# Performance work log

Hardware: AMD Instinct MI355X
Metric: run time of the kernel (lower is better)

Reference implementation:

```python
import jax, jax.numpy as jnp
import numpy as np

EPS = 1e-3  # keras LayerNormalization default epsilon
H = 12     # number_of_heads


def _layer_norm(x, gamma, beta):
    mu = jnp.mean(x, axis=-1, keepdims=True)
    var = jnp.mean(jnp.square(x - mu), axis=-1, keepdims=True)
    return (x - mu) * jax.lax.rsqrt(var + EPS) * gamma + beta


def _gelu(x):
    return jax.nn.gelu(x, approximate=False)  # keras 'gelu' default is erf-based


def setup_inputs():
    key = jax.random.key(0)
    B, N, E, F, Fe = 8, 1024, 16384, 96, 32
    ks = jax.random.split(key, 20)
    def dense(k, din, dout):
        return jax.random.normal(k, (din, dout), jnp.float32) / np.float32(np.sqrt(din))
    return {
        "nodes": jax.random.normal(ks[0], (B, N, F), jnp.float32),
        "edge_features": jax.random.normal(ks[1], (B, E, Fe), jnp.float32),
        "edges": jax.random.randint(ks[2], (B, E, 2), 0, N),
        "edge_weights": jax.random.uniform(ks[3], (B, E, 1), jnp.float32),
        "edge_dropout": jnp.ones((B, E, 2), jnp.float32),
        # message layer: Dense(F) on concat([src,dst,edge_feat]) + GELU + LayerNorm
        "Wm": dense(ks[4], 2 * F + Fe, F), "bm": jnp.zeros((F,), jnp.float32),
        "gm": jnp.ones((F,), jnp.float32), "betam": jnp.zeros((F,), jnp.float32),
        # gated MHSA on concat([nodes, aggregated]) (2F -> F) + GELU + LayerNorm
        "Wq": dense(ks[5], 2 * F, F), "bq": jnp.zeros((F,), jnp.float32),
        "Wk": dense(ks[6], 2 * F, F), "bk": jnp.zeros((F,), jnp.float32),
        "Wv": dense(ks[7], 2 * F, F), "bv": jnp.zeros((F,), jnp.float32),
        "Wg": dense(ks[8], 2 * F, F), "bg": jnp.zeros((F,), jnp.float32),
        "Wo": dense(ks[9], F, F), "bo": jnp.zeros((F,), jnp.float32),
        "gu": jnp.ones((F,), jnp.float32), "betau": jnp.zeros((F,), jnp.float32),
    }


def reference(nodes, edge_features, edges, edge_weights, edge_dropout,
              Wm, bm, gm, betam, Wq, bq, Wk, bk, Wv, bv, Wg, bg, Wo, bo, gu, betau):
    B, N, F = nodes.shape
    E = edges.shape[1]
    # gather both endpoint features per edge: [B, E, 2F]
    gathered = jnp.take_along_axis(nodes, edges.reshape(B, 2 * E, 1), axis=1)
    msg_in = jnp.concatenate([gathered.reshape(B, E, 2 * F), edge_features], axis=-1)
    messages = _layer_norm(_gelu(msg_in @ Wm + bm), gm, betam)        # [B,E,F]
    weighted_messages = messages * edge_weights                        # [B,E,F]
    # batched scatter-sum onto target node edges[...,1], gated by dropout[...,1]
    contrib = weighted_messages * edge_dropout[..., 1:2]
    seg_ids = (edges[..., 1] + jnp.arange(B, dtype=edges.dtype)[:, None] * N).reshape(-1)
    aggregated = jax.ops.segment_sum(contrib.reshape(B * E, F), seg_ids,
                                     num_segments=B * N).reshape(B, N, F)
    # gated multi-head self-attention over concat(nodes, aggregated)
    x = jnp.concatenate([nodes, aggregated], axis=-1)                  # [B,N,2F]
    d = F // H
    def split_heads(y):
        return y.reshape(B, N, H, d).transpose(0, 2, 1, 3)             # [B,H,N,d]
    q = split_heads(x @ Wq + bq)
    k = split_heads(x @ Wk + bk)
    v = split_heads(x @ Wv + bv)
    gate = jax.nn.sigmoid(split_heads(x @ Wg + bg))
    scores = jnp.einsum("bhqd,bhkd->bhqk", q, k) / jnp.sqrt(jnp.float32(d))
    att = jnp.einsum("bhqk,bhkd->bhqd", jax.nn.softmax(scores, axis=-1), v) * gate
    att = att.transpose(0, 2, 1, 3).reshape(B, N, F)
    updated_nodes = _layer_norm(_gelu(att @ Wo + bo), gu, betau)
    return updated_nodes, weighted_messages, edges, edge_weights, edge_dropout
```

## Files before the change

### kernel.cpp

```cpp
#include <hip/hip_runtime.h>
#include <hip/hip_bf16.h>

#define BB 8
#define NN 1024
#define EE 16384
#define FF 96
#define FE 32
#define NH 12
#define DD 8
#define KM 224
#define KX 192
#define TE 64
#define BK 32

__device__ __forceinline__ float gelu_erf(float x){
    return 0.5f * x * (1.0f + erff(x * 0.70710678118654752f));
}

__device__ __forceinline__ int load_idx(const int* __restrict__ p, int i){
    int v = p[i];
    if (!((unsigned)v < 1024u)) v = (int)__int_as_float(v);
    return min(max(v, 0), NN-1);
}

__global__ __launch_bounds__(256) void hist_kernel(
    const int* __restrict__ edges, int* __restrict__ cnt)
{
    const int i = blockIdx.x*blockDim.x + threadIdx.x;
    if (i < BB*EE){
        const int b = i >> 14;
        const int dst = load_idx(edges, 2*i+1);
        atomicAdd(&cnt[b*NN + dst], 1);
    }
}

__global__ __launch_bounds__(1024) void scan_kernel(
    const int* __restrict__ cnt, int* __restrict__ rowstart, int* __restrict__ cursor)
{
    const int b = blockIdx.x;
    const int t = threadIdx.x;
    __shared__ int s[NN];
    const int v = cnt[b*NN + t];
    s[t] = v;
    __syncthreads();
    for (int off = 1; off < NN; off <<= 1){
        int u = (t >= off) ? s[t-off] : 0;
        __syncthreads();
        s[t] += u;
        __syncthreads();
    }
    const int ex = s[t] - v + b*EE;
    rowstart[b*NN + t] = ex;
    cursor[b*NN + t]   = ex;
}

__global__ __launch_bounds__(256) void scatter_kernel(
    const int* __restrict__ edges, int* __restrict__ cursor, int* __restrict__ elist)
{
    const int i = blockIdx.x*blockDim.x + threadIdx.x;
    if (i < BB*EE){
        const int b = i >> 14;
        const int dst = load_idx(edges, 2*i+1);
        const int pos = atomicAdd(&cursor[b*NN + dst], 1);
        elist[pos] = i;
    }
}

__global__ __launch_bounds__(256) void node_proj_kernel(
    const float* __restrict__ nodes, const float* __restrict__ Wm,
    float* __restrict__ P1, float* __restrict__ P2)
{
    const int rt  = blockIdx.x;
    const int m   = blockIdx.y;
    const int tid = threadIdx.x;
    const int tx  = tid & 15;
    const int ty  = tid >> 4;
    const int r0  = rt * TE;

    const float* W = Wm + (size_t)(m ? FF : 0) * FF;
    float* out     = m ? P2 : P1;

    __shared__ float Xs[TE][BK+4];
    __shared__ float Ws[BK][FF];

    float acc[4][6];
    #pragma unroll
    for (int a=0;a<4;++a)
        #pragma unroll
        for (int c=0;c<6;++c) acc[a][c] = 0.f;

    const int e_st = tid >> 2;
    const int kk0  = (tid & 3) * 8;

    for (int c = 0; c < 3; ++c){
        __syncthreads();
        {
            const float4* src = (const float4*)(W + (size_t)c*BK*FF);
            float4* dst = (float4*)&Ws[0][0];
            dst[tid      ] = src[tid      ];
            dst[tid + 256] = src[tid + 256];
            dst[tid + 512] = src[tid + 512];
        }
        {
            const float* rp = nodes + (size_t)(r0 + e_st)*FF + c*BK;
            *(float4*)&Xs[e_st][kk0    ] = *(const float4*)(rp + kk0);
            *(float4*)&Xs[e_st][kk0 + 4] = *(const float4*)(rp + kk0 + 4);
        }
        __syncthreads();
        #pragma unroll 4
        for (int kk = 0; kk < BK; ++kk){
            float2 w01 = *(const float2*)&Ws[kk][6*tx    ];
            float2 w23 = *(const float2*)&Ws[kk][6*tx + 2];
            float2 w45 = *(const float2*)&Ws[kk][6*tx + 4];
            float xv[4];
            #pragma unroll
            for (int ei=0; ei<4; ++ei) xv[ei] = Xs[ty + 16*ei][kk];
            #pragma unroll
            for (int ei=0; ei<4; ++ei){
                acc[ei][0] += xv[ei]*w01.x;  acc[ei][1] += xv[ei]*w01.y;
                acc[ei][2] += xv[ei]*w23.x;  acc[ei][3] += xv[ei]*w23.y;
                acc[ei][4] += xv[ei]*w45.x;  acc[ei][5] += xv[ei]*w45.y;
            }
        }
    }

    #pragma unroll
    for (int ei = 0; ei < 4; ++ei){
        const int row = r0 + ty + 16*ei;
        float* __restrict__ orow = out + (size_t)row*FF + 6*tx;
        #pragma unroll
        for (int jj=0; jj<6; ++jj) orow[jj] = acc[ei][jj];
    }
}

__global__ __launch_bounds__(256) void edge_msg2_kernel(
    const float* __restrict__ P1, const float* __restrict__ P2,
    const float* __restrict__ ef,
    const int*  __restrict__ edges, const float* __restrict__ ew,
    const float* __restrict__ Wm, const float* __restrict__ bm,
    const float* __restrict__ gm, const float* __restrict__ betam,
    float* __restrict__ wm_out)
{
    const int bid = blockIdx.x;
    const int tid = threadIdx.x;
    const int tx  = tid & 15;
    const int ty  = tid >> 4;
    const int be0 = bid * TE;
    const int b   = be0 >> 14;

    __shared__ float Xs[TE][BK+4];
    __shared__ float Ws[BK][FF];
    __shared__ int   eidx[TE*2];
    __shared__ float ewS[TE];
    __shared__ float bmS[FF], gmS[FF], betamS[FF];

    if (tid < TE*2){
        int v = edges[(size_t)be0*2 + tid];
        if (!((unsigned)v < 1024u)) v = (int)__int_as_float(v);
        eidx[tid] = min(max(v, 0), NN-1);
    }
    if (tid < TE) ewS[tid] = ew[be0 + tid];
    if (tid < FF){ bmS[tid] = bm[tid]; gmS[tid] = gm[tid]; betamS[tid] = betam[tid]; }

    float acc[4][6];
    #pragma unroll
    for (int a=0;a<4;++a)
        #pragma unroll
        for (int c=0;c<6;++c) acc[a][c] = 0.f;

    const int e_st = tid >> 2;
    const int kk0  = (tid & 3) * 8;

    {
        const float4* src = (const float4*)(Wm + (size_t)KX*FF);
        float4* dst = (float4*)&Ws[0][0];
        dst[tid      ] = src[tid      ];
        dst[tid + 256] = src[tid + 256];
        dst[tid + 512] = src[tid + 512];
    }
    {
        const float* rp = ef + (size_t)(be0 + e_st)*FE;
        *(float4*)&Xs[e_st][kk0    ] = *(const float4*)(rp + kk0);
        *(float4*)&Xs[e_st][kk0 + 4] = *(const float4*)(rp + kk0 + 4);
    }
    __syncthreads();
    #pragma unroll 4
    for (int kk = 0; kk < BK; ++kk){
        float2 w01 = *(const float2*)&Ws[kk][6*tx    ];
        float2 w23 = *(const float2*)&Ws[kk][6*tx + 2];
        float2 w45 = *(const float2*)&Ws[kk][6*tx + 4];
        float xv[4];
        #pragma unroll
        for (int ei=0; ei<4; ++ei) xv[ei] = Xs[ty + 16*ei][kk];
        #pragma unroll
        for (int ei=0; ei<4; ++ei){
            acc[ei][0] += xv[ei]*w01.x;  acc[ei][1] += xv[ei]*w01.y;
            acc[ei][2] += xv[ei]*w23.x;  acc[ei][3] += xv[ei]*w23.y;
            acc[ei][4] += xv[ei]*w45.x;  acc[ei][5] += xv[ei]*w45.y;
        }
    }

    float add[4][6];
    #pragma unroll
    for (int ei = 0; ei < 4; ++ei){
        const int el = ty + 16*ei;
        const int sn = eidx[2*el];
        const int dn = eidx[2*el+1];
        const float2* p1 = (const float2*)(P1 + (size_t)(b*NN + sn)*FF + 6*tx);
        const float2* p2 = (const float2*)(P2 + (size_t)(b*NN + dn)*FF + 6*tx);
        const float2 a0 = p1[0], a1 = p1[1], a2 = p1[2];
        const float2 b0 = p2[0], b1 = p2[1], b2 = p2[2];
        add[ei][0] = a0.x + b0.x;  add[ei][1] = a0.y + b0.y;
        add[ei][2] = a1.x + b1.x;  add[ei][3] = a1.y + b1.y;
        add[ei][4] = a2.x + b2.x;  add[ei][5] = a2.y + b2.y;
    }

    #pragma unroll
    for (int ei = 0; ei < 4; ++ei){
        const int el = ty + 16*ei;
        float h[6]; float psum = 0.f;
        #pragma unroll
        for (int jj=0; jj<6; ++jj){
            h[jj] = gelu_erf(acc[ei][jj] + add[ei][jj] + bmS[6*tx + jj]);
            psum += h[jj];
        }
        #pragma unroll
        for (int m=1; m<16; m<<=1) psum += __shfl_xor(psum, m, 16);
        const float mu = psum * (1.f/FF);
        float vsum = 0.f;
        #pragma unroll
        for (int jj=0; jj<6; ++jj){ float d = h[jj]-mu; vsum += d*d; }
        #pragma unroll
        for (int m=1; m<16; m<<=1) vsum += __shfl_xor(vsum, m, 16);
        const float rstd = rsqrtf(vsum*(1.f/FF) + 1e-3f);

        const float w = ewS[el];
        float* __restrict__ wrow = wm_out + (size_t)(be0 + el)*FF + 6*tx;
        #pragma unroll
        for (int jj=0; jj<6; ++jj)
            wrow[jj] = ((h[jj]-mu)*rstd*gmS[6*tx+jj] + betamS[6*tx+jj]) * w;
    }
}

__global__ __launch_bounds__(96) void gather_kernel(
    const float* __restrict__ wm_out, const float* __restrict__ ed,
    const int* __restrict__ elist, const int* __restrict__ rowstart,
    const int* __restrict__ cnt, float* __restrict__ agg)
{
    const int bn = blockIdx.x;
    const int t  = threadIdx.x;
    const int beg = rowstart[bn];
    const int num = cnt[bn];
    float sum = 0.f;
    for (int i = 0; i < num; ++i){
        const int be = elist[beg + i];
        const float coeff = ed[2*(size_t)be + 1];
        sum += wm_out[(size_t)be*FF + t] * coeff;
    }
    agg[(size_t)bn*FF + t] = sum;
}

__global__ __launch_bounds__(256) void qkvg_kernel(
    const float* __restrict__ nodes, const float* __restrict__ agg,
    const float* __restrict__ Wq, const float* __restrict__ bq,
    const float* __restrict__ Wk, const float* __restrict__ bk,
    const float* __restrict__ Wv, const float* __restrict__ bv,
    const float* __restrict__ Wg, const float* __restrict__ bg,
    float* __restrict__ qo, float* __restrict__ ko,
    float* __restrict__ vo, float* __restrict__ go)
{
    const int rt  = blockIdx.x;
    const int m   = blockIdx.y;
    const int tid = threadIdx.x;
    const int tx  = tid & 15;
    const int ty  = tid >> 4;
    const int r0  = rt * TE;

    const float* W    = (m==0)?Wq:(m==1)?Wk:(m==2)?Wv:Wg;
    const float* bias = (m==0)?bq:(m==1)?bk:(m==2)?bv:bg;
    float* out        = (m==0)?qo:(m==1)?ko:(m==2)?vo:go;

    __shared__ float Xs[TE][BK+4];
    __shared__ float Ws[BK][FF];
    __shared__ float bS[FF];
    if (tid < FF) bS[tid] = bias[tid];

    float acc[4][6];
    #pragma unroll
    for (int a=0;a<4;++a)
        #pragma unroll
        for (int c=0;c<6;++c) acc[a][c] = 0.f;

    const int e_st = tid >> 2;
    const int kk0  = (tid & 3) * 8;

    for (int c = 0; c < 6; ++c){
        __syncthreads();
        {
            const float4* src = (const float4*)(W + (size_t)c*BK*FF);
            float4* dst = (float4*)&Ws[0][0];
            dst[tid      ] = src[tid      ];
            dst[tid + 256] = src[tid + 256];
            dst[tid + 512] = src[tid + 512];
        }
        {
            const float* rp = (c < 3)
                ? nodes + (size_t)(r0 + e_st)*FF + c*BK
                : agg   + (size_t)(r0 + e_st)*FF + (c-3)*BK;
            *(float4*)&Xs[e_st][kk0    ] = *(const float4*)(rp + kk0);
            *(float4*)&Xs[e_st][kk0 + 4] = *(const float4*)(rp + kk0 + 4);
        }
        __syncthreads();
        #pragma unroll 4
        for (int kk = 0; kk < BK; ++kk){
            float2 w01 = *(const float2*)&Ws[kk][6*tx    ];
            float2 w23 = *(const float2*)&Ws[kk][6*tx + 2];
            float2 w45 = *(const float2*)&Ws[kk][6*tx + 4];
            float xv[4];
            #pragma unroll
            for (int ei=0; ei<4; ++ei) xv[ei] = Xs[ty + 16*ei][kk];
            #pragma unroll
            for (int ei=0; ei<4; ++ei){
                acc[ei][0] += xv[ei]*w01.x;  acc[ei][1] += xv[ei]*w01.y;
                acc[ei][2] += xv[ei]*w23.x;  acc[ei][3] += xv[ei]*w23.y;
                acc[ei][4] += xv[ei]*w45.x;  acc[ei][5] += xv[ei]*w45.y;
            }
        }
    }

    #pragma unroll
    for (int ei = 0; ei < 4; ++ei){
        const int row = r0 + ty + 16*ei;
        float* __restrict__ orow = out + (size_t)row*FF + 6*tx;
        #pragma unroll
        for (int jj=0; jj<6; ++jj) orow[jj] = acc[ei][jj] + bS[6*tx + jj];
    }
}

__global__ __launch_bounds__(256) void attn_kernel(
    const float* __restrict__ q, const float* __restrict__ k,
    const float* __restrict__ v, const float* g,
    float* att)
{
    const int blk = blockIdx.x;
    const int qt = blk & 15;
    const int h  = (blk >> 4) % NH;
    const int b  = blk / (16*NH);
    const int tid  = threadIdx.x;
    const int lane = tid & 63;
    const int w    = tid >> 6;
    const int r    = lane & 15;
    const int s    = lane >> 4;
    const int qrow = qt*64 + w*16 + r;
    const size_t base = (size_t)(b*NN)*FF + h*DD;

    __shared__ float Ks[128][12];
    __shared__ float Vs[128][12];

    float qr[DD];
    const float* qp = q + base + (size_t)qrow*FF;
    #pragma unroll
    for (int i=0;i<DD;++i) qr[i] = qp[i] * 0.35355339059327373f;

    float m = -1e30f, l = 0.f, o[DD];
    #pragma unroll
    for (int i=0;i<DD;++i) o[i] = 0.f;

    const int skey  = tid >> 1;
    const int shalf = (tid & 1) * 4;

    for (int kc = 0; kc < NN; kc += 128){
        __syncthreads();
        {
            const float* kp = k + base + (size_t)(kc + skey)*FF + shalf;
            const float* vp = v + base + (size_t)(kc + skey)*FF + shalf;
            *(float4*)&Ks[skey][shalf] = *(const float4*)kp;
            *(float4*)&Vs[skey][shalf] = *(const float4*)vp;
        }
        __syncthreads();
        #pragma unroll
        for (int gidx = 0; gidx < 4; ++gidx){
            float sc[8];
            #pragma unroll
            for (int jj = 0; jj < 8; ++jj){
                const int key = 32*gidx + 4*jj + s;
                float4 k0 = *(const float4*)&Ks[key][0];
                float4 k1 = *(const float4*)&Ks[key][4];
                sc[jj] = qr[0]*k0.x + qr[1]*k0.y + qr[2]*k0.z + qr[3]*k0.w
                       + qr[4]*k1.x + qr[5]*k1.y + qr[6]*k1.z + qr[7]*k1.w;
            }
            const float g01 = fmaxf(sc[0], sc[1]), g23 = fmaxf(sc[2], sc[3]);
            const float g45 = fmaxf(sc[4], sc[5]), g67 = fmaxf(sc[6], sc[7]);
            const float gmax = fmaxf(fmaxf(g01, g23), fmaxf(g45, g67));
            if (gmax > m + 8.f){
                const float c = __expf(m - gmax);
                l *= c;
                #pragma unroll
                for (int i=0;i<DD;++i) o[i] *= c;
                m = gmax;
            }
            #pragma unroll
            for (int jj = 0; jj < 8; ++jj){
                const int key = 32*gidx + 4*jj + s;
                float4 v0 = *(const float4*)&Vs[key][0];
                float4 v1 = *(const float4*)&Vs[key][4];
                const float p = __expf(sc[jj] - m);
                l += p;
                o[0] += p*v0.x;  o[1] += p*v0.y;
                o[2] += p*v0.z;  o[3] += p*v0.w;
                o[4] += p*v1.x;  o[5] += p*v1.y;
                o[6] += p*v1.z;  o[7] += p*v1.w;
            }
        }
    }

    #pragma unroll
    for (int mask = 16; mask <= 32; mask <<= 1){
        const float m2 = __shfl_xor(m, mask);
        const float l2 = __shfl_xor(l, mask);
        float o2[DD];
        #pragma unroll
        for (int i=0;i<DD;++i) o2[i] = __shfl_xor(o[i], mask);
        const float M  = fmaxf(m, m2);
        const float c1 = __expf(m - M);
        const float c2 = __expf(m2 - M);
        l = l*c1 + l2*c2;
        #pragma unroll
        for (int i=0;i<DD;++i) o[i] = o[i]*c1 + o2[i]*c2;
        m = M;
    }

    if (s == 0){
        const float inv = 1.f / l;
        const float* gp = g + base + (size_t)qrow*FF;
        float* ap = att + base + (size_t)qrow*FF;
        #pragma unroll
        for (int i=0;i<DD;++i){
            const float gate = 1.f/(1.f + __expf(-gp[i]));
            ap[i] = o[i]*inv*gate;
        }
    }
}

__global__ __launch_bounds__(256) void out_kernel(
    const float* __restrict__ att, const float* __restrict__ Wo, const float* __restrict__ bo,
    const float* __restrict__ gu, const float* __restrict__ betau,
    float* __restrict__ out0)
{
    const int rt  = blockIdx.x;
    const int tid = threadIdx.x;
    const int tx  = tid & 15;
    const int ty  = tid >> 4;
    const int r0  = rt * TE;

    __shared__ float Xs[TE][BK+4];
    __shared__ float Ws[BK][FF];
    __shared__ float boS[FF], guS[FF], beS[FF];
    if (tid < FF){ boS[tid] = bo[tid]; guS[tid] = gu[tid]; beS[tid] = betau[tid]; }

    float acc[4][6];
    #pragma unroll
    for (int a=0;a<4;++a)
        #pragma unroll
        for (int c=0;c<6;++c) acc[a][c] = 0.f;

    const int e_st = tid >> 2;
    const int kk0  = (tid & 3) * 8;

    for (int c = 0; c < 3; ++c){
        __syncthreads();
        {
            const float4* src = (const float4*)(Wo + (size_t)c*BK*FF);
            float4* dst = (float4*)&Ws[0][0];
            dst[tid      ] = src[tid      ];
            dst[tid + 256] = src[tid + 256];
            dst[tid + 512] = src[tid + 512];
        }
        {
            const float* rp = att + (size_t)(r0 + e_st)*FF + c*BK;
            *(float4*)&Xs[e_st][kk0    ] = *(const float4*)(rp + kk0);
            *(float4*)&Xs[e_st][kk0 + 4] = *(const float4*)(rp + kk0 + 4);
        }
        __syncthreads();
        #pragma unroll 4
        for (int kk = 0; kk < BK; ++kk){
            float2 w01 = *(const float2*)&Ws[kk][6*tx    ];
            float2 w23 = *(const float2*)&Ws[kk][6*tx + 2];
            float2 w45 = *(const float2*)&Ws[kk][6*tx + 4];
            float xv[4];
            #pragma unroll
            for (int ei=0; ei<4; ++ei) xv[ei] = Xs[ty + 16*ei][kk];
            #pragma unroll
            for (int ei=0; ei<4; ++ei){
                acc[ei][0] += xv[ei]*w01.x;  acc[ei][1] += xv[ei]*w01.y;
                acc[ei][2] += xv[ei]*w23.x;  acc[ei][3] += xv[ei]*w23.y;
                acc[ei][4] += xv[ei]*w45.x;  acc[ei][5] += xv[ei]*w45.y;
            }
        }
    }

    #pragma unroll
    for (int ei = 0; ei < 4; ++ei){
        const int row = r0 + ty + 16*ei;
        float h[6]; float psum = 0.f;
        #pragma unroll
        for (int jj=0; jj<6; ++jj){
            h[jj] = gelu_erf(acc[ei][jj] + boS[6*tx + jj]);
            psum += h[jj];
        }
        #pragma unroll
        for (int m=1; m<16; m<<=1) psum += __shfl_xor(psum, m, 16);
        const float mu = psum * (1.f/FF);
        float vsum = 0.f;
        #pragma unroll
        for (int jj=0; jj<6; ++jj){ float d = h[jj]-mu; vsum += d*d; }
        #pragma unroll
        for (int m=1; m<16; m<<=1) vsum += __shfl_xor(vsum, m, 16);
        const float rstd = rsqrtf(vsum*(1.f/FF) + 1e-3f);
        float* __restrict__ orow = out0 + (size_t)row*FF + 6*tx;
        #pragma unroll
        for (int jj=0; jj<6; ++jj)
            orow[jj] = (h[jj]-mu)*rstd*guS[6*tx+jj] + beS[6*tx+jj];
    }
}

__global__ void passthrough_kernel(const int* __restrict__ edges,
    const float* __restrict__ ew, const float* __restrict__ ed,
    float* __restrict__ o_edges, float* __restrict__ o_ew, float* __restrict__ o_ed)
{
    const int i = blockIdx.x*blockDim.x + threadIdx.x;
    const int NE2 = BB*EE*2;
    const int NW  = BB*EE;
    if (i < NE2)                 o_edges[i] = (float)load_idx(edges, i);
    else if (i < NE2+NW)         o_ew[i-NE2] = ew[i-NE2];
    else if (i < NE2+NW+NE2)     o_ed[i-NE2-NW] = ed[i-NE2-NW];
}

extern "C" void kernel_launch(void* const* d_in, const int* in_sizes, int n_in,
                              void* d_out, int out_size, void* d_ws, size_t ws_size,
                              hipStream_t stream) {
    int i_nodes=-1, i_ef=-1, i_edges=-1, i_ed=-1, i_ew=-1, i_Wm=-1, i_Wo=-1;
    int i_W4[4]; int nW4=0;
    int i_v96[10]; int nv96=0;
    for (int i = 0; i < n_in; ++i){
        const int s = in_sizes[i];
        if      (s == 786432)  i_nodes = i;
        else if (s == 4194304) i_ef = i;
        else if (s == 262144)  { if (i_edges < 0) i_edges = i; else i_ed = i; }
        else if (s == 131072)  i_ew = i;
        else if (s == 21504)   i_Wm = i;
        else if (s == 18432)   { if (nW4 < 4) i_W4[nW4++] = i; }
        else if (s == 9216)    i_Wo = i;
        else if (s == 96)      { if (nv96 < 10) i_v96[nv96++] = i; }
    }
    const float* nodes = (const float*)d_in[i_nodes];
    const float* ef    = (const float*)d_in[i_ef];
    const int*   edges = (const int*)d_in[i_edges];
    const float* ew    = (const float*)d_in[i_ew];
    const float* ed    = (const float*)d_in[i_ed];
    const float* Wm = (const float*)d_in[i_Wm];
    const float* Wq = (const float*)d_in[i_W4[0]];
    const float* Wk = (const float*)d_in[i_W4[1]];
    const float* Wv = (const float*)d_in[i_W4[2]];
    const float* Wg = (const float*)d_in[i_W4[3]];
    const float* Wo = (const float*)d_in[i_Wo];
    const float* bm    = (const float*)d_in[i_v96[0]];
    const float* gm    = (const float*)d_in[i_v96[1]];
    const float* betam = (const float*)d_in[i_v96[2]];
    const float* bq    = (const float*)d_in[i_v96[3]];
    const float* bk    = (const float*)d_in[i_v96[4]];
    const float* bv    = (const float*)d_in[i_v96[5]];
    const float* bg    = (const float*)d_in[i_v96[6]];
    const float* bo    = (const float*)d_in[i_v96[7]];
    const float* gu    = (const float*)d_in[i_v96[8]];
    const float* betau = (const float*)d_in[i_v96[9]];

    float* outp = (float*)d_out;
    const size_t ROWS  = (size_t)BB*NN*FF;
    const size_t WMSZ  = (size_t)BB*EE*FF;
    const size_t NE2   = (size_t)BB*EE*2;
    const size_t NW    = (size_t)BB*EE;
    float* out_un    = outp;
    float* out_wm    = outp + ROWS;
    float* out_edges = outp + ROWS + WMSZ;
    float* out_ew    = outp + ROWS + WMSZ + NE2;
    float* out_ed    = outp + ROWS + WMSZ + NE2 + NW;

    float* ws  = (float*)d_ws;
    float* agg = ws;
    float* qo  = ws + 1*ROWS;
    float* ko  = ws + 2*ROWS;
    float* vo  = ws + 3*ROWS;
    float* go  = ws + 4*ROWS;
    float* att = go;
    float* P1  = qo;
    float* P2  = ko;
    int* ints      = (int*)(ws + 5*ROWS);
    int* cnt       = ints;
    int* rowstart  = ints + BB*NN;
    int* cursor    = ints + 2*BB*NN;
    int* elist     = ints + 3*BB*NN;

    hipMemsetAsync(cnt, 0, BB*NN*sizeof(int), stream);

    hist_kernel<<<(BB*EE+255)/256, 256, 0, stream>>>(edges, cnt);
    scan_kernel<<<BB, NN, 0, stream>>>(cnt, rowstart, cursor);
    scatter_kernel<<<(BB*EE+255)/256, 256, 0, stream>>>(edges, cursor, elist);

    dim3 npgrid((BB*NN)/TE, 2);
    node_proj_kernel<<<npgrid, 256, 0, stream>>>(nodes, Wm, P1, P2);

    edge_msg2_kernel<<<(BB*EE)/TE, 256, 0, stream>>>(P1, P2, ef, edges, ew,
                                               Wm, bm, gm, betam, out_wm);
    gather_kernel<<<BB*NN, 96, 0, stream>>>(out_wm, ed, elist, rowstart, cnt, agg);

    dim3 qgrid((BB*NN)/TE, 4);
    qkvg_kernel<<<qgrid, 256, 0, stream>>>(nodes, agg, Wq, bq, Wk, bk, Wv, bv,
                                           Wg, bg, qo, ko, vo, go);
    attn_kernel<<<BB*NH*16, 256, 0, stream>>>(qo, ko, vo, go, att);
    out_kernel<<<(BB*NN)/TE, 256, 0, stream>>>(att, Wo, bo, gu, betau, out_un);

    const int npass = (int)(NE2 + NW + NE2);
    passthrough_kernel<<<(npass+255)/256, 256, 0, stream>>>(edges, ew, ed,
                                               out_edges, out_ew, out_ed);
}
```

Before: 311.6 us.

## Fuse segment-sum into edge kernel via atomics; exp2 softmax and register-prefetched K/V

After: 514.0 us. 65.0% more time.

```diff
diff --git a/kernel.cpp b/kernel.cpp
--- a/kernel.cpp
+++ b/kernel.cpp
@@ -13,6 +13,12 @@
 #define TE 64
 #define BK 32
 
+#if __has_builtin(__builtin_amdgcn_exp2f)
+#define EXP2(x) __builtin_amdgcn_exp2f(x)
+#else
+#define EXP2(x) exp2f(x)
+#endif
+
 __device__ __forceinline__ float gelu_erf(float x){
     return 0.5f * x * (1.0f + erff(x * 0.70710678118654752f));
 }
@@ -21,49 +27,6 @@
     int v = p[i];
     if (!((unsigned)v < 1024u)) v = (int)__int_as_float(v);
     return min(max(v, 0), NN-1);
-}
-
-__global__ __launch_bounds__(256) void hist_kernel(
-    const int* __restrict__ edges, int* __restrict__ cnt)
-{
-    const int i = blockIdx.x*blockDim.x + threadIdx.x;
-    if (i < BB*EE){
-        const int b = i >> 14;
-        const int dst = load_idx(edges, 2*i+1);
-        atomicAdd(&cnt[b*NN + dst], 1);
-    }
-}
-
-__global__ __launch_bounds__(1024) void scan_kernel(
-    const int* __restrict__ cnt, int* __restrict__ rowstart, int* __restrict__ cursor)
-{
-    const int b = blockIdx.x;
-    const int t = threadIdx.x;
-    __shared__ int s[NN];
-    const int v = cnt[b*NN + t];
-    s[t] = v;
-    __syncthreads();
-    for (int off = 1; off < NN; off <<= 1){
-        int u = (t >= off) ? s[t-off] : 0;
-        __syncthreads();
-        s[t] += u;
-        __syncthreads();
-    }
-    const int ex = s[t] - v + b*EE;
-    rowstart[b*NN + t] = ex;
-    cursor[b*NN + t]   = ex;
-}
-
-__global__ __launch_bounds__(256) void scatter_kernel(
-    const int* __restrict__ edges, int* __restrict__ cursor, int* __restrict__ elist)
-{
-    const int i = blockIdx.x*blockDim.x + threadIdx.x;
-    if (i < BB*EE){
-        const int b = i >> 14;
-        const int dst = load_idx(edges, 2*i+1);
-        const int pos = atomicAdd(&cursor[b*NN + dst], 1);
-        elist[pos] = i;
-    }
 }
 
 __global__ __launch_bounds__(256) void node_proj_kernel(
@@ -137,9 +100,10 @@
     const float* __restrict__ P1, const float* __restrict__ P2,
     const float* __restrict__ ef,
     const int*  __restrict__ edges, const float* __restrict__ ew,
+    const float* __restrict__ ed,
     const float* __restrict__ Wm, const float* __restrict__ bm,
     const float* __restrict__ gm, const float* __restrict__ betam,
-    float* __restrict__ wm_out)
+    float* __restrict__ wm_out, float* __restrict__ agg)
 {
     const int bid = blockIdx.x;
     const int tid = threadIdx.x;
@@ -152,6 +116,7 @@
     __shared__ float Ws[BK][FF];
     __shared__ int   eidx[TE*2];
     __shared__ float ewS[TE];
+    __shared__ float edS[TE];
     __shared__ float bmS[FF], gmS[FF], betamS[FF];
 
     if (tid < TE*2){
@@ -159,7 +124,10 @@
         if (!((unsigned)v < 1024u)) v = (int)__int_as_float(v);
         eidx[tid] = min(max(v, 0), NN-1);
     }
-    if (tid < TE) ewS[tid] = ew[be0 + tid];
+    if (tid < TE){
+        ewS[tid] = ew[be0 + tid];
+        edS[tid] = ed[(size_t)(be0 + tid)*2 + 1];
+    }
     if (tid < FF){ bmS[tid] = bm[tid]; gmS[tid] = gm[tid]; betamS[tid] = betam[tid]; }
 
     float acc[4][6];
@@ -235,29 +203,17 @@
         const float rstd = rsqrtf(vsum*(1.f/FF) + 1e-3f);
 
         const float w = ewS[el];
+        const float coeff = edS[el];
+        const int   dn = eidx[2*el+1];
         float* __restrict__ wrow = wm_out + (size_t)(be0 + el)*FF + 6*tx;
-        #pragma unroll
-        for (int jj=0; jj<6; ++jj)
-            wrow[jj] = ((h[jj]-mu)*rstd*gmS[6*tx+jj] + betamS[6*tx+jj]) * w;
-    }
-}
-
-__global__ __launch_bounds__(96) void gather_kernel(
-    const float* __restrict__ wm_out, const float* __restrict__ ed,
-    const int* __restrict__ elist, const int* __restrict__ rowstart,
-    const int* __restrict__ cnt, float* __restrict__ agg)
-{
-    const int bn = blockIdx.x;
-    const int t  = threadIdx.x;
-    const int beg = rowstart[bn];
-    const int num = cnt[bn];
-    float sum = 0.f;
-    for (int i = 0; i < num; ++i){
-        const int be = elist[beg + i];
-        const float coeff = ed[2*(size_t)be + 1];
-        sum += wm_out[(size_t)be*FF + t] * coeff;
-    }
-    agg[(size_t)bn*FF + t] = sum;
+        float* __restrict__ arow = agg + (size_t)(b*NN + dn)*FF + 6*tx;
+        #pragma unroll
+        for (int jj=0; jj<6; ++jj){
+            const float wv = ((h[jj]-mu)*rstd*gmS[6*tx+jj] + betamS[6*tx+jj]) * w;
+            wrow[jj] = wv;
+            atomicAdd(&arow[jj], wv * coeff);
+        }
+    }
 }
 
 __global__ __launch_bounds__(256) void qkvg_kernel(
@@ -360,7 +316,7 @@
     float qr[DD];
     const float* qp = q + base + (size_t)qrow*FF;
     #pragma unroll
-    for (int i=0;i<DD;++i) qr[i] = qp[i] * 0.35355339059327373f;
+    for (int i=0;i<DD;++i) qr[i] = qp[i] * 0.51010300101462254f;
 
     float m = -1e30f, l = 0.f, o[DD];
     #pragma unroll
@@ -369,15 +325,17 @@
     const int skey  = tid >> 1;
     const int shalf = (tid & 1) * 4;
 
-    for (int kc = 0; kc < NN; kc += 128){
-        __syncthreads();
-        {
-            const float* kp = k + base + (size_t)(kc + skey)*FF + shalf;
-            const float* vp = v + base + (size_t)(kc + skey)*FF + shalf;
-            *(float4*)&Ks[skey][shalf] = *(const float4*)kp;
-            *(float4*)&Vs[skey][shalf] = *(const float4*)vp;
-        }
-        __syncthreads();
+    float4 kreg = *(const float4*)(k + base + (size_t)skey*FF + shalf);
+    float4 vreg = *(const float4*)(v + base + (size_t)skey*FF + shalf);
+
+    for (int t = 0; t < 8; ++t){
+        *(float4*)&Ks[skey][shalf] = kreg;
+        *(float4*)&Vs[skey][shalf] = vreg;
+        __syncthreads();
+        if (t < 7){
+            kreg = *(const float4*)(k + base + (size_t)((t+1)*128 + skey)*FF + shalf);
+            vreg = *(const float4*)(v + base + (size_t)((t+1)*128 + skey)*FF + shalf);
+        }
         #pragma unroll
         for (int gidx = 0; gidx < 4; ++gidx){
             float sc[8];
@@ -392,8 +350,8 @@
             const float g01 = fmaxf(sc[0], sc[1]), g23 = fmaxf(sc[2], sc[3]);
             const float g45 = fmaxf(sc[4], sc[5]), g67 = fmaxf(sc[6], sc[7]);
             const float gmax = fmaxf(fmaxf(g01, g23), fmaxf(g45, g67));
-            if (gmax > m + 8.f){
-                const float c = __expf(m - gmax);
+            if (gmax > m + 11.5f){
+                const float c = EXP2(m - gmax);
                 l *= c;
                 #pragma unroll
                 for (int i=0;i<DD;++i) o[i] *= c;
@@ -404,7 +362,7 @@
                 const int key = 32*gidx + 4*jj + s;
                 float4 v0 = *(const float4*)&Vs[key][0];
                 float4 v1 = *(const float4*)&Vs[key][4];
-                const float p = __expf(sc[jj] - m);
+                const float p = EXP2(sc[jj] - m);
                 l += p;
                 o[0] += p*v0.x;  o[1] += p*v0.y;
                 o[2] += p*v0.z;  o[3] += p*v0.w;
@@ -412,6 +370,7 @@
                 o[6] += p*v1.z;  o[7] += p*v1.w;
             }
         }
+        if (t < 7) __syncthreads();
     }
 
     #pragma unroll
@@ -422,8 +381,8 @@
         #pragma unroll
         for (int i=0;i<DD;++i) o2[i] = __shfl_xor(o[i], mask);
         const float M  = fmaxf(m, m2);
-        const float c1 = __expf(m - M);
-        const float c2 = __expf(m2 - M);
+        const float c1 = EXP2(m - M);
+        const float c2 = EXP2(m2 - M);
         l = l*c1 + l2*c2;
         #pragma unroll
         for (int i=0;i<DD;++i) o[i] = o[i]*c1 + o2[i]*c2;
@@ -595,24 +554,14 @@
     float* att = go;
     float* P1  = qo;
     float* P2  = ko;
-    int* ints      = (int*)(ws + 5*ROWS);
-    int* cnt       = ints;
-    int* rowstart  = ints + BB*NN;
-    int* cursor    = ints + 2*BB*NN;
-    int* elist     = ints + 3*BB*NN;
-
-    hipMemsetAsync(cnt, 0, BB*NN*sizeof(int), stream);
-
-    hist_kernel<<<(BB*EE+255)/256, 256, 0, stream>>>(edges, cnt);
-    scan_kernel<<<BB, NN, 0, stream>>>(cnt, rowstart, cursor);
-    scatter_kernel<<<(BB*EE+255)/256, 256, 0, stream>>>(edges, cursor, elist);
+
+    hipMemsetAsync(agg, 0, ROWS*sizeof(float), stream);
 
     dim3 npgrid((BB*NN)/TE, 2);
     node_proj_kernel<<<npgrid, 256, 0, stream>>>(nodes, Wm, P1, P2);
 
-    edge_msg2_kernel<<<(BB*EE)/TE, 256, 0, stream>>>(P1, P2, ef, edges, ew,
-                                               Wm, bm, gm, betam, out_wm);
-    gather_kernel<<<BB*NN, 96, 0, stream>>>(out_wm, ed, elist, rowstart, cnt, agg);
+    edge_msg2_kernel<<<(BB*EE)/TE, 256, 0, stream>>>(P1, P2, ef, edges, ew, ed,
+                                               Wm, bm, gm, betam, out_wm, agg);
 
     dim3 qgrid((BB*NN)/TE, 4);
     qkvg_kernel<<<qgrid, 256, 0, stream>>>(nodes, agg, Wq, bq, Wk, bk, Wv, bv,
```
